# Performance work log

Measured on AMD Instinct MI355X. Metric: run time of the kernel, lower is better.

Reference implementation:

```python
import jax, jax.numpy as jnp
import numpy as np

ETYPES = ((0, 2), (4, 6))  # per-metapath edge-type indices into the doubled r_vec table
ALPHA = 3.0


def celu3(x):
    return jax.nn.celu(x, alpha=ALPHA)


def cmul(a, b):
    # complex multiply, last dim = (real, imag)
    re = a[..., 0] * b[..., 0] - a[..., 1] * b[..., 1]
    im = a[..., 0] * b[..., 1] + a[..., 1] * b[..., 0]
    return jnp.stack([re, im], axis=-1)


def setup_inputs() -> dict:
    key = jax.random.key(0)
    ks = jax.random.split(key, 10)
    N, H, heads, M, E, P = 50000, 64, 4, 2, 250000, 3
    R, FH = 4, 128
    D = heads * H
    return {
        "features": jax.random.normal(ks[0], (N, H), jnp.float32),
        "r_vec": jax.random.normal(ks[1], (R, H // 2, 2), jnp.float32),
        "attn1_w": jax.random.normal(ks[2], (heads, H), jnp.float32) * 0.1,
        "attn2": jax.random.normal(ks[3], (1, heads, H), jnp.float32) * 0.1,
        "fw1": jax.random.normal(ks[4], (2 * FH, D), jnp.float32) * 0.05,
        "fb1": jnp.zeros((2 * FH,), jnp.float32),
        "fw2": jax.random.normal(ks[5], (FH, 2 * FH), jnp.float32) * 0.05,
        "fb2": jnp.zeros((FH,), jnp.float32),
        "fw3": jax.random.normal(ks[6], (1, FH), jnp.float32) * 0.05,
        "instances": jax.random.randint(ks[7], (M, E, P), 0, N, jnp.int32),
    }


def reference(features, r_vec, attn1_w, attn2, fw1, fb1, fw2, fb2, fw3, instances):
    N, H = features.shape
    M, E, P = instances.shape
    heads = attn1_w.shape[0]
    # unit-modulus rotations + conjugates: [2R, H/2, 2], even=r, odd=conj(r)
    rv = r_vec / jnp.linalg.norm(r_vec, axis=2, keepdims=True)
    conj = rv * jnp.array([1.0, -1.0], rv.dtype)
    rv2 = jnp.stack([rv, conj], axis=1).reshape(-1, H // 2, 2)

    per_path = []
    for m in range(M):
        inst = instances[m]  # [E, P]
        # backward cumulative rotation: final_r[i] = prod_{j>=i} r_{etype[j]}, final_r[P-1]=1
        ident = jnp.stack([jnp.ones(H // 2, rv.dtype), jnp.zeros(H // 2, rv.dtype)], axis=-1)
        frs = [ident]
        for i in range(P - 2, -1, -1):
            frs.insert(0, cmul(frs[0], rv2[ETYPES[m][i]]))
        fr = jnp.stack(frs)  # [P, H/2, 2]
        # gather features along metapath and rotate (last position rotated by identity)
        edata = features[inst].reshape(E, P, H // 2, 2)
        rot = cmul(edata, fr[None])
        me = jnp.mean(rot.reshape(E, P, H), axis=1)  # [E, H]
        se = celu3(me) * jax.nn.sigmoid(me)  # gated metapath embedding
        eft = celu3(se)  # same across heads in original (tiled)
        seg = inst[:, 0]  # target node per instance
        a1 = celu3(features[seg] @ attn1_w.T)  # [E, heads]
        a2 = jnp.einsum('eh,kh->ek', eft, attn2[0])  # [E, heads]
        a = celu3(a1 + a2)
        # segment softmax over each node's instance set
        amax = jax.ops.segment_max(a, seg, num_segments=N)
        ex = jnp.exp(a - amax[seg])
        den = jax.ops.segment_sum(ex, seg, num_segments=N)
        attn = ex / den[seg]  # [E, heads]
        hsum = jax.ops.segment_sum(attn[:, :, None] * eft[:, None, :], seg, num_segments=N)
        per_path.append(celu3(hsum).reshape(N, heads * H))  # empty nodes -> 0

    z = jnp.stack(per_path, axis=1)  # [N, M, D]
    t = celu3(z @ fw1.T + fb1)
    t = celu3(t @ fw2.T + fb2)
    w = (t @ fw3.T).mean(axis=0)  # [M, 1]
    beta = jax.nn.softmax(w, axis=0)
    out = (beta * z).sum(axis=1)  # [N, D]
    return out
```

## Files before the change

kernel.cpp:

```cpp
#include <hip/hip_runtime.h>
#include <hip/hip_bf16.h>

typedef unsigned short u16;
typedef unsigned int   u32;
typedef short bf16x8 __attribute__((ext_vector_type(8)));
typedef float f32x4  __attribute__((ext_vector_type(4)));

#define CAP 64

__device__ inline float b2f(u16 u){ return __builtin_bit_cast(float, (u32)u << 16); }
__device__ inline u16 f2b(float f){
  u32 x = __builtin_bit_cast(u32, f);
  x += 0x7fffu + ((x >> 16) & 1u);
  return (u16)(x >> 16);
}
__device__ inline u32 pk2(float lo, float hi){
  float2 f; f.x = lo; f.y = hi;
  __hip_bfloat162 h = __float22bfloat162_rn(f);
  u32 r; __builtin_memcpy(&r, &h, 4);
  return r;
}
__device__ inline void up2(u32 u, float& lo, float& hi){
  lo = __builtin_bit_cast(float, u << 16);
  hi = __builtin_bit_cast(float, u & 0xffff0000u);
}
__device__ inline float fexp(float x){ return __expf(x); }
__device__ inline float celu3(float x){
  return x > 0.f ? x : 3.f * (__expf(x * (1.f/3.f)) - 1.f);
}
__device__ inline float sigm(float x){ return 1.f / (1.f + __expf(-x)); }

__global__ __launch_bounds__(256) void conv_kernel(
    const float* __restrict__ src, u16* __restrict__ dst, int n8)
{
  int i = blockIdx.x * 256 + threadIdx.x;
  if (i >= n8) return;
  float4 a = ((const float4*)src)[2*i], b = ((const float4*)src)[2*i + 1];
  uint4 o;
  o.x = pk2(a.x, a.y);
  o.y = pk2(a.z, a.w);
  o.z = pk2(b.x, b.y);
  o.w = pk2(b.z, b.w);
  ((uint4*)dst)[i] = o;
}

__global__ __launch_bounds__(256) void a1_kernel(
    const float* __restrict__ feat, const float* __restrict__ attn1,
    u16* __restrict__ featb, float* __restrict__ a1c, int N)
{
  __shared__ float w1s[256];
  int t = threadIdx.x;
  w1s[t] = attn1[t];
  __syncthreads();
  int g = t >> 4, l = t & 15;
  int n = blockIdx.x * 16 + g;
  if (n >= N) return;
  float4 x = ((const float4*)feat)[(size_t)n*16 + l];
  uint2 o;
  o.x = pk2(x.x, x.y);
  o.y = pk2(x.z, x.w);
  ((uint2*)featb)[(size_t)n*16 + l] = o;
  float d[4];
  #pragma unroll
  for (int k = 0; k < 4; ++k){
    int wb = k*64 + l*4;
    d[k] = x.x*w1s[wb] + x.y*w1s[wb+1] + x.z*w1s[wb+2] + x.w*w1s[wb+3];
  }
  #pragma unroll
  for (int off = 8; off; off >>= 1){
    #pragma unroll
    for (int k = 0; k < 4; ++k) d[k] += __shfl_xor(d[k], off);
  }
  if (l == 0){
    float4 av;
    av.x = celu3(d[0]); av.y = celu3(d[1]);
    av.z = celu3(d[2]); av.w = celu3(d[3]);
    ((float4*)a1c)[n] = av;
  }
}

__global__ void fr_kernel(const float* __restrict__ rvec, float* __restrict__ fr){
  int c = threadIdx.x;
  if (c >= 32) return;
  for (int m = 0; m < 2; ++m){
    float ar = rvec[(2*m)*64 + c*2],   ai = rvec[(2*m)*64 + c*2 + 1];
    float br = rvec[(2*m+1)*64 + c*2], bi = rvec[(2*m+1)*64 + c*2 + 1];
    float na = rsqrtf(ar*ar + ai*ai); ar *= na; ai *= na;
    float nb = rsqrtf(br*br + bi*bi); br *= nb; bi *= nb;
    float* f = fr + m*128;
    f[c*2]        = br*ar - bi*ai;
    f[c*2 + 1]    = br*ai + bi*ar;
    f[64 + c*2]   = br;
    f[64 + c*2+1] = bi;
  }
}

__global__ __launch_bounds__(256) void edge_kernel(
    const u16* __restrict__ featb, const int* __restrict__ inst,
    const float* __restrict__ fr, const float* __restrict__ a1c,
    const float* __restrict__ attn2, u16* __restrict__ eft,
    float* __restrict__ a_ws, int* __restrict__ cnt, int* __restrict__ bucket,
    int E, int N)
{
  __shared__ float frs[128];
  __shared__ float w2s[256];
  int m = blockIdx.y;
  int t = threadIdx.x;
  if (t < 128) frs[t] = fr[m*128 + t];
  w2s[t] = attn2[t];
  __syncthreads();

  int g = t >> 4, l = t & 15;
  int e = blockIdx.x * 16 + g;
  if (e >= E) return;
  int base = (m*E + e)*3;
  int i0 = inst[base], i1 = inst[base+1], i2 = inst[base+2];

  const uint2* fb = (const uint2*)featb;
  uint2 v0 = fb[(size_t)i0*16 + l];
  uint2 v1 = fb[(size_t)i1*16 + l];
  uint2 v2 = fb[(size_t)i2*16 + l];
  float f0[4], f1[4], f2v[4];
  up2(v0.x, f0[0], f0[1]); up2(v0.y, f0[2], f0[3]);
  up2(v1.x, f1[0], f1[1]); up2(v1.y, f1[2], f1[3]);
  up2(v2.x, f2v[0], f2v[1]); up2(v2.y, f2v[2], f2v[3]);

  float4 R0 = *(const float4*)&frs[4*l];
  float4 R1 = *(const float4*)&frs[64 + 4*l];

  float mre0 = (f0[0]*R0.x - f0[1]*R0.y + f1[0]*R1.x - f1[1]*R1.y + f2v[0]) * (1.f/3.f);
  float mim0 = (f0[0]*R0.y + f0[1]*R0.x + f1[0]*R1.y + f1[1]*R1.x + f2v[1]) * (1.f/3.f);
  float mre1 = (f0[2]*R0.z - f0[3]*R0.w + f1[2]*R1.z - f1[3]*R1.w + f2v[2]) * (1.f/3.f);
  float mim1 = (f0[2]*R0.w + f0[3]*R0.z + f1[2]*R1.w + f1[3]*R1.z + f2v[3]) * (1.f/3.f);

  float ef[4], s;
  s = celu3(mre0) * sigm(mre0); ef[0] = celu3(s);
  s = celu3(mim0) * sigm(mim0); ef[1] = celu3(s);
  s = celu3(mre1) * sigm(mre1); ef[2] = celu3(s);
  s = celu3(mim1) * sigm(mim1); ef[3] = celu3(s);

  uint2 uo;
  uo.x = pk2(ef[0], ef[1]);
  uo.y = pk2(ef[2], ef[3]);
  ((uint2*)eft)[(size_t)(m*E + e)*16 + l] = uo;

  float d2[4];
  #pragma unroll
  for (int k = 0; k < 4; ++k){
    int wb = k*64 + l*4;
    d2[k] = ef[0]*w2s[wb] + ef[1]*w2s[wb+1] + ef[2]*w2s[wb+2] + ef[3]*w2s[wb+3];
  }
  #pragma unroll
  for (int off = 8; off; off >>= 1){
    #pragma unroll
    for (int k = 0; k < 4; ++k) d2[k] += __shfl_xor(d2[k], off);
  }
  if (l == 0){
    float4 a1v = ((const float4*)a1c)[i0];
    float4 av;
    av.x = celu3(a1v.x + d2[0]);
    av.y = celu3(a1v.y + d2[1]);
    av.z = celu3(a1v.z + d2[2]);
    av.w = celu3(a1v.w + d2[3]);
    ((float4*)a_ws)[m*E + e] = av;
    int pos = atomicAdd(&cnt[m*N + i0], 1);
    if (pos < CAP) bucket[(size_t)(m*N + i0)*CAP + pos] = e;
  }
}

__global__ __launch_bounds__(256) void seg_kernel(
    const float* __restrict__ a_ws, const u16* __restrict__ eft,
    const int* __restrict__ cnt, const int* __restrict__ bucket,
    u16* __restrict__ z, int E, int N)
{
  int m = blockIdx.y;
  int n = blockIdx.x * 4 + (threadIdx.x >> 6);
  if (n >= N) return;
  int lane = threadIdx.x & 63;
  int sidx = m*N + n;
  int deg = cnt[sidx]; if (deg > CAP) deg = CAP;

  float h0=0.f, h1=0.f, h2=0.f, h3=0.f;
  float d0=0.f, d1=0.f, d2=0.f, d3=0.f;
  if (deg > 0){
    const int* bk = bucket + (size_t)sidx * CAP;
    size_t ebase = (size_t)m * E;

    int e = (lane < deg) ? bk[lane] : 0;
    float w0 = 0.f, w1 = 0.f, w2 = 0.f, w3 = 0.f;
    if (lane < deg){
      float4 av = ((const float4*)a_ws)[ebase + e];
      w0 = fexp(av.x); w1 = fexp(av.y); w2 = fexp(av.z); w3 = fexp(av.w);
    }

    const u16* ep = eft + ebase*64;
    for (int j = 0; j < deg; ++j){
      int   ej  = __shfl(e,  j);
      float a0j = __shfl(w0, j), a1j = __shfl(w1, j);
      float a2j = __shfl(w2, j), a3j = __shfl(w3, j);
      float ev = b2f(ep[(size_t)ej*64 + lane]);
      h0 += a0j*ev; h1 += a1j*ev; h2 += a2j*ev; h3 += a3j*ev;
      d0 += a0j;    d1 += a1j;    d2 += a2j;    d3 += a3j;
    }
    h0 /= d0; h1 /= d1; h2 /= d2; h3 /= d3;
  }
  u16* zr = z + (size_t)sidx*256 + lane;
  zr[0]   = f2b(celu3(h0));
  zr[64]  = f2b(celu3(h1));
  zr[128] = f2b(celu3(h2));
  zr[192] = f2b(celu3(h3));
}

__global__ __launch_bounds__(256, 4) void mlp_kernel(
    const u16* __restrict__ z, const u16* __restrict__ fw1b, const float* __restrict__ fb1,
    const u16* __restrict__ fw2b, const float* __restrict__ fb2, const float* __restrict__ fw3,
    float* __restrict__ wacc, int rows, int N)
{
  __shared__ u16 buf[64][264];
  __shared__ float fw3s[128];
  __shared__ float sArr[64];
  u16 (*t2t)[136] = (u16 (*)[136])&buf[0][0];
  int tid = threadIdx.x;
  int row0 = blockIdx.x * 64;

  if (tid < 128) fw3s[tid] = fw3[tid];

  const uint4* zg = (const uint4*)z;
  #pragma unroll
  for (int it = 0; it < 8; ++it){
    int idx = it*256 + tid;
    int row = idx >> 5;
    int c8  = idx & 31;
    uint4 v = make_uint4(0u,0u,0u,0u);
    int gr = row0 + row;
    if (gr < rows) v = zg[(size_t)gr*32 + c8];
    *(uint4*)&buf[row][c8*8] = v;
  }
  __syncthreads();

  int wv = tid >> 6, lane = tid & 63, lr = lane & 15, quad = lane >> 4;
  f32x4 zero4 = {0.f, 0.f, 0.f, 0.f};

  f32x4 acc[4][4];
  #pragma unroll
  for (int a = 0; a < 4; ++a)
    #pragma unroll
    for (int b = 0; b < 4; ++b) acc[a][b] = zero4;

  const u16* wb1 = fw1b + (size_t)(wv*64 + lr)*256 + quad*8;
  bf16x8 bfr[4], bnx[4];
  #pragma unroll
  for (int nt = 0; nt < 4; ++nt) bfr[nt] = *(const bf16x8*)(wb1 + nt*16*256);
  #pragma unroll
  for (int ks = 0; ks < 8; ++ks){
    if (ks < 7){
      #pragma unroll
      for (int nt = 0; nt < 4; ++nt)
        bnx[nt] = *(const bf16x8*)(wb1 + nt*16*256 + (ks+1)*32);
    }
    #pragma unroll
    for (int mt = 0; mt < 4; ++mt){
      bf16x8 af = *(const bf16x8*)&buf[mt*16 + lr][ks*32 + quad*8];
      #pragma unroll
      for (int nt = 0; nt < 4; ++nt)
        acc[mt][nt] = __builtin_amdgcn_mfma_f32_16x16x32_bf16(af, bfr[nt], acc[mt][nt], 0, 0, 0);
    }
    #pragma unroll
    for (int nt = 0; nt < 4; ++nt) bfr[nt] = bnx[nt];
  }
  __syncthreads();
  #pragma unroll
  for (int nt = 0; nt < 4; ++nt){
    int col = wv*64 + nt*16 + lr;
    float bias = fb1[col];
    #pragma unroll
    for (int mt = 0; mt < 4; ++mt)
      #pragma unroll
      for (int ri = 0; ri < 4; ++ri){
        int row = mt*16 + quad*4 + ri;
        buf[row][col] = f2b(celu3(acc[mt][nt][ri] + bias));
      }
  }
  __syncthreads();

  f32x4 acc2[4][2];
  #pragma unroll
  for (int a = 0; a < 4; ++a){ acc2[a][0] = zero4; acc2[a][1] = zero4; }
  const u16* wb2 = fw2b + (size_t)(wv*32 + lr)*256 + quad*8;
  bf16x8 cfr[2], cnx[2];
  cfr[0] = *(const bf16x8*)(wb2);
  cfr[1] = *(const bf16x8*)(wb2 + 16*256);
  #pragma unroll
  for (int ks = 0; ks < 8; ++ks){
    if (ks < 7){
      cnx[0] = *(const bf16x8*)(wb2 + (ks+1)*32);
      cnx[1] = *(const bf16x8*)(wb2 + 16*256 + (ks+1)*32);
    }
    #pragma unroll
    for (int mt = 0; mt < 4; ++mt){
      bf16x8 af = *(const bf16x8*)&buf[mt*16 + lr][ks*32 + quad*8];
      acc2[mt][0] = __builtin_amdgcn_mfma_f32_16x16x32_bf16(af, cfr[0], acc2[mt][0], 0, 0, 0);
      acc2[mt][1] = __builtin_amdgcn_mfma_f32_16x16x32_bf16(af, cfr[1], acc2[mt][1], 0, 0, 0);
    }
    cfr[0] = cnx[0]; cfr[1] = cnx[1];
  }
  __syncthreads();
  #pragma unroll
  for (int nt = 0; nt < 2; ++nt){
    int col = wv*32 + nt*16 + lr;
    float bias = fb2[col];
    #pragma unroll
    for (int mt = 0; mt < 4; ++mt)
      #pragma unroll
      for (int ri = 0; ri < 4; ++ri)
        t2t[mt*16 + quad*4 + ri][col] = f2b(celu3(acc2[mt][nt][ri] + bias));
  }
  __syncthreads();

  int r = tid >> 2, q = tid & 3;
  float p = 0.f;
  #pragma unroll
  for (int j = 0; j < 32; ++j){
    int jj = q*32 + j;
    p += b2f(t2t[r][jj]) * fw3s[jj];
  }
  p += __shfl_xor(p, 1);
  p += __shfl_xor(p, 2);
  if (q == 0) sArr[r] = p;
  __syncthreads();

  if (tid < 64){
    int gr = row0 + tid;
    float s  = (gr < rows) ? sArr[tid] : 0.f;
    float s0 = (gr < N) ? s : 0.f;
    float s1 = (gr < N) ? 0.f : s;
    #pragma unroll
    for (int off = 32; off; off >>= 1){
      s0 += __shfl_xor(s0, off);
      s1 += __shfl_xor(s1, off);
    }
    if (tid == 0){
      atomicAdd(&wacc[0], s0);
      atomicAdd(&wacc[1], s1);
    }
  }
}

__global__ void beta_kernel(float* __restrict__ wacc, float invN){
  if (threadIdx.x == 0 && blockIdx.x == 0){
    float w0 = wacc[0]*invN, w1 = wacc[1]*invN;
    float mx = fmaxf(w0, w1);
    float e0 = __expf(w0 - mx), e1 = __expf(w1 - mx);
    float s = e0 + e1;
    wacc[2] = e0 / s;
    wacc[3] = e1 / s;
  }
}

__global__ __launch_bounds__(256) void out_kernel(
    const u16* __restrict__ z, const float* __restrict__ wacc,
    float* __restrict__ out, int total)
{
  int idx = blockIdx.x * 256 + threadIdx.x;
  if (idx*8 >= total) return;
  float b0 = wacc[2], b1 = wacc[3];
  uint4 u0 = ((const uint4*)z)[idx];
  uint4 u1 = ((const uint4*)z)[(total >> 3) + idx];
  float a0,a1v,c0,c1;
  float4 o;
  up2(u0.x, a0, a1v); up2(u1.x, c0, c1);
  o.x = b0*a0 + b1*c0; o.y = b0*a1v + b1*c1;
  up2(u0.y, a0, a1v); up2(u1.y, c0, c1);
  o.z = b0*a0 + b1*c0; o.w = b0*a1v + b1*c1;
  ((float4*)out)[idx*2] = o;
  up2(u0.z, a0, a1v); up2(u1.z, c0, c1);
  o.x = b0*a0 + b1*c0; o.y = b0*a1v + b1*c1;
  up2(u0.w, a0, a1v); up2(u1.w, c0, c1);
  o.z = b0*a0 + b1*c0; o.w = b0*a1v + b1*c1;
  ((float4*)out)[idx*2 + 1] = o;
}

extern "C" void kernel_launch(void* const* d_in, const int* in_sizes, int n_in,
                              void* d_out, int out_size, void* d_ws, size_t ws_size,
                              hipStream_t stream)
{
  (void)n_in; (void)out_size; (void)ws_size;
  const float* feat  = (const float*)d_in[0];
  const float* rvec  = (const float*)d_in[1];
  const float* attn1 = (const float*)d_in[2];
  const float* attn2 = (const float*)d_in[3];
  const float* fw1   = (const float*)d_in[4];
  const float* fb1   = (const float*)d_in[5];
  const float* fw2   = (const float*)d_in[6];
  const float* fb2   = (const float*)d_in[7];
  const float* fw3   = (const float*)d_in[8];
  const int*   inst  = (const int*)d_in[9];

  int N = in_sizes[0] / 64;
  int E = in_sizes[9] / 6;

  char* ws = (char*)d_ws;
  u16*   z      = (u16*)ws;                            size_t zB = (size_t)2*N*256*2;
  u16*   eft    = (u16*)(ws + zB);                     size_t eB = (size_t)2*E*64*2;
  float* a_ws   = (float*)(ws + zB + eB);              size_t aB = (size_t)2*E*4*4;
  int*   bucket = (int*)(ws + zB + eB + aB);           size_t bB = (size_t)2*N*CAP*4;
  int*   cnt    = (int*)(ws + zB + eB + aB + bB);      size_t cB = (size_t)2*N*4;
  u16*   featb  = (u16*)(ws + zB + eB + aB + bB + cB); size_t fB = (size_t)N*64*2;
  float* a1c    = (float*)(ws + zB + eB + aB + bB + cB + fB);  size_t a1B = (size_t)N*4*4;
  u16*   fw1b   = (u16*)(ws + zB + eB + aB + bB + cB + fB + a1B);
  u16*   fw2b   = fw1b + 256*256;
  float* fr     = (float*)(fw2b + 128*256);
  float* wacc   = fr + 256;

  hipMemsetAsync(cnt, 0, cB, stream);
  hipMemsetAsync(wacc, 0, 2*sizeof(float), stream);

  a1_kernel<<<(N + 15)/16, 256, 0, stream>>>(feat, attn1, featb, a1c, N);
  conv_kernel<<<(256*256/8 + 255)/256, 256, 0, stream>>>(fw1, fw1b, 256*256/8);
  conv_kernel<<<(128*256/8 + 255)/256, 256, 0, stream>>>(fw2, fw2b, 128*256/8);
  fr_kernel<<<1, 64, 0, stream>>>(rvec, fr);
  edge_kernel<<<dim3((E + 15)/16, 2), 256, 0, stream>>>(
      featb, inst, fr, a1c, attn2, eft, a_ws, cnt, bucket, E, N);
  seg_kernel<<<dim3((N + 3)/4, 2), 256, 0, stream>>>(a_ws, eft, cnt, bucket, z, E, N);
  mlp_kernel<<<(2*N + 63)/64, 256, 0, stream>>>(z, fw1b, fb1, fw2b, fb2, fw3, wacc, 2*N, N);
  beta_kernel<<<1, 64, 0, stream>>>(wacc, 1.f/(float)N);
  out_kernel<<<((N*256/8) + 255)/256, 256, 0, stream>>>(z, wacc, (float*)d_out, N*256);
}
```

Before: 302.2 us.

## Shrink MLP tiles to 32 rows, fuse fw3 dot into registers, spread atomics

The MLP kernel now processes 32 rows per block instead of 64 and targets 6 blocks per CU. It drops the software prefetch of weight fragments and computes the final fw3 dot product straight from MFMA accumulators with shuffle reductions, which removes the second LDS round-trip and two barriers. The global atomics are spread over 64 slots per metapath, and beta_kernel reduces those slots. The cost is twice as many blocks, each reloading the weights from L2, and less latency hiding on the weight loads.

After: 310.2 us. 2.6% more time.

```diff
diff --git a/kernel.cpp b/kernel.cpp
--- a/kernel.cpp
+++ b/kernel.cpp
@@ -211,23 +211,22 @@
   zr[192] = f2b(celu3(h3));
 }
 
-__global__ __launch_bounds__(256, 4) void mlp_kernel(
+__global__ __launch_bounds__(256, 6) void mlp_kernel(
     const u16* __restrict__ z, const u16* __restrict__ fw1b, const float* __restrict__ fb1,
     const u16* __restrict__ fw2b, const float* __restrict__ fb2, const float* __restrict__ fw3,
-    float* __restrict__ wacc, int rows, int N)
-{
-  __shared__ u16 buf[64][264];
+    float* __restrict__ waccP, int rows, int N)
+{
+  __shared__ u16 buf[32][264];
   __shared__ float fw3s[128];
-  __shared__ float sArr[64];
-  u16 (*t2t)[136] = (u16 (*)[136])&buf[0][0];
+  __shared__ float sPart[4][32];
   int tid = threadIdx.x;
-  int row0 = blockIdx.x * 64;
+  int row0 = blockIdx.x * 32;
 
   if (tid < 128) fw3s[tid] = fw3[tid];
 
   const uint4* zg = (const uint4*)z;
   #pragma unroll
-  for (int it = 0; it < 8; ++it){
+  for (int it = 0; it < 4; ++it){
     int idx = it*256 + tid;
     int row = idx >> 5;
     int c8  = idx & 31;
@@ -241,32 +240,26 @@
   int wv = tid >> 6, lane = tid & 63, lr = lane & 15, quad = lane >> 4;
   f32x4 zero4 = {0.f, 0.f, 0.f, 0.f};
 
-  f32x4 acc[4][4];
-  #pragma unroll
-  for (int a = 0; a < 4; ++a)
+  f32x4 acc[2][4];
+  #pragma unroll
+  for (int a = 0; a < 2; ++a)
     #pragma unroll
     for (int b = 0; b < 4; ++b) acc[a][b] = zero4;
 
   const u16* wb1 = fw1b + (size_t)(wv*64 + lr)*256 + quad*8;
-  bf16x8 bfr[4], bnx[4];
-  #pragma unroll
-  for (int nt = 0; nt < 4; ++nt) bfr[nt] = *(const bf16x8*)(wb1 + nt*16*256);
   #pragma unroll
   for (int ks = 0; ks < 8; ++ks){
-    if (ks < 7){
-      #pragma unroll
-      for (int nt = 0; nt < 4; ++nt)
-        bnx[nt] = *(const bf16x8*)(wb1 + nt*16*256 + (ks+1)*32);
-    }
-    #pragma unroll
-    for (int mt = 0; mt < 4; ++mt){
+    bf16x8 bfr[4];
+    #pragma unroll
+    for (int nt = 0; nt < 4; ++nt)
+      bfr[nt] = *(const bf16x8*)(wb1 + nt*16*256 + ks*32);
+    #pragma unroll
+    for (int mt = 0; mt < 2; ++mt){
       bf16x8 af = *(const bf16x8*)&buf[mt*16 + lr][ks*32 + quad*8];
       #pragma unroll
       for (int nt = 0; nt < 4; ++nt)
         acc[mt][nt] = __builtin_amdgcn_mfma_f32_16x16x32_bf16(af, bfr[nt], acc[mt][nt], 0, 0, 0);
     }
-    #pragma unroll
-    for (int nt = 0; nt < 4; ++nt) bfr[nt] = bnx[nt];
   }
   __syncthreads();
   #pragma unroll
@@ -274,7 +267,7 @@
     int col = wv*64 + nt*16 + lr;
     float bias = fb1[col];
     #pragma unroll
-    for (int mt = 0; mt < 4; ++mt)
+    for (int mt = 0; mt < 2; ++mt)
       #pragma unroll
       for (int ri = 0; ri < 4; ++ri){
         int row = mt*16 + quad*4 + ri;
@@ -283,77 +276,89 @@
   }
   __syncthreads();
 
-  f32x4 acc2[4][2];
-  #pragma unroll
-  for (int a = 0; a < 4; ++a){ acc2[a][0] = zero4; acc2[a][1] = zero4; }
+  f32x4 acc2[2][2];
+  #pragma unroll
+  for (int a = 0; a < 2; ++a){ acc2[a][0] = zero4; acc2[a][1] = zero4; }
   const u16* wb2 = fw2b + (size_t)(wv*32 + lr)*256 + quad*8;
-  bf16x8 cfr[2], cnx[2];
-  cfr[0] = *(const bf16x8*)(wb2);
-  cfr[1] = *(const bf16x8*)(wb2 + 16*256);
   #pragma unroll
   for (int ks = 0; ks < 8; ++ks){
-    if (ks < 7){
-      cnx[0] = *(const bf16x8*)(wb2 + (ks+1)*32);
-      cnx[1] = *(const bf16x8*)(wb2 + 16*256 + (ks+1)*32);
-    }
-    #pragma unroll
-    for (int mt = 0; mt < 4; ++mt){
+    bf16x8 cfr[2];
+    cfr[0] = *(const bf16x8*)(wb2 + ks*32);
+    cfr[1] = *(const bf16x8*)(wb2 + 16*256 + ks*32);
+    #pragma unroll
+    for (int mt = 0; mt < 2; ++mt){
       bf16x8 af = *(const bf16x8*)&buf[mt*16 + lr][ks*32 + quad*8];
       acc2[mt][0] = __builtin_amdgcn_mfma_f32_16x16x32_bf16(af, cfr[0], acc2[mt][0], 0, 0, 0);
       acc2[mt][1] = __builtin_amdgcn_mfma_f32_16x16x32_bf16(af, cfr[1], acc2[mt][1], 0, 0, 0);
     }
-    cfr[0] = cnx[0]; cfr[1] = cnx[1];
-  }
-  __syncthreads();
+  }
+
+  float ps[2][4];
+  #pragma unroll
+  for (int mt = 0; mt < 2; ++mt)
+    #pragma unroll
+    for (int ri = 0; ri < 4; ++ri) ps[mt][ri] = 0.f;
   #pragma unroll
   for (int nt = 0; nt < 2; ++nt){
     int col = wv*32 + nt*16 + lr;
     float bias = fb2[col];
-    #pragma unroll
-    for (int mt = 0; mt < 4; ++mt)
+    float w3 = fw3s[col];
+    #pragma unroll
+    for (int mt = 0; mt < 2; ++mt)
       #pragma unroll
       for (int ri = 0; ri < 4; ++ri)
-        t2t[mt*16 + quad*4 + ri][col] = f2b(celu3(acc2[mt][nt][ri] + bias));
-  }
-  __syncthreads();
-
-  int r = tid >> 2, q = tid & 3;
-  float p = 0.f;
-  #pragma unroll
-  for (int j = 0; j < 32; ++j){
-    int jj = q*32 + j;
-    p += b2f(t2t[r][jj]) * fw3s[jj];
-  }
-  p += __shfl_xor(p, 1);
-  p += __shfl_xor(p, 2);
-  if (q == 0) sArr[r] = p;
-  __syncthreads();
-
-  if (tid < 64){
+        ps[mt][ri] += celu3(acc2[mt][nt][ri] + bias) * w3;
+  }
+  #pragma unroll
+  for (int off = 8; off; off >>= 1)
+    #pragma unroll
+    for (int mt = 0; mt < 2; ++mt)
+      #pragma unroll
+      for (int ri = 0; ri < 4; ++ri)
+        ps[mt][ri] += __shfl_xor(ps[mt][ri], off);
+  if (lr == 0){
+    #pragma unroll
+    for (int mt = 0; mt < 2; ++mt)
+      #pragma unroll
+      for (int ri = 0; ri < 4; ++ri)
+        sPart[wv][mt*16 + quad*4 + ri] = ps[mt][ri];
+  }
+  __syncthreads();
+
+  if (tid < 32){
+    float s = sPart[0][tid] + sPart[1][tid] + sPart[2][tid] + sPart[3][tid];
     int gr = row0 + tid;
-    float s  = (gr < rows) ? sArr[tid] : 0.f;
+    if (gr >= rows) s = 0.f;
     float s0 = (gr < N) ? s : 0.f;
     float s1 = (gr < N) ? 0.f : s;
     #pragma unroll
-    for (int off = 32; off; off >>= 1){
+    for (int off = 16; off; off >>= 1){
       s0 += __shfl_xor(s0, off);
       s1 += __shfl_xor(s1, off);
     }
     if (tid == 0){
-      atomicAdd(&wacc[0], s0);
-      atomicAdd(&wacc[1], s1);
+      int slot = blockIdx.x & 63;
+      atomicAdd(&waccP[slot],      s0);
+      atomicAdd(&waccP[64 + slot], s1);
     }
   }
 }
 
 __global__ void beta_kernel(float* __restrict__ wacc, float invN){
-  if (threadIdx.x == 0 && blockIdx.x == 0){
-    float w0 = wacc[0]*invN, w1 = wacc[1]*invN;
+  int t = threadIdx.x;
+  float s0 = wacc[t], s1 = wacc[64 + t];
+  #pragma unroll
+  for (int off = 32; off; off >>= 1){
+    s0 += __shfl_xor(s0, off);
+    s1 += __shfl_xor(s1, off);
+  }
+  if (t == 0){
+    float w0 = s0*invN, w1 = s1*invN;
     float mx = fmaxf(w0, w1);
     float e0 = __expf(w0 - mx), e1 = __expf(w1 - mx);
     float s = e0 + e1;
-    wacc[2] = e0 / s;
-    wacc[3] = e1 / s;
+    wacc[128] = e0 / s;
+    wacc[129] = e1 / s;
   }
 }
 
@@ -363,7 +368,7 @@
 {
   int idx = blockIdx.x * 256 + threadIdx.x;
   if (idx*8 >= total) return;
-  float b0 = wacc[2], b1 = wacc[3];
+  float b0 = wacc[128], b1 = wacc[129];
   uint4 u0 = ((const uint4*)z)[idx];
   uint4 u1 = ((const uint4*)z)[(total >> 3) + idx];
   float a0,a1v,c0,c1;
@@ -413,7 +418,7 @@
   float* wacc   = fr + 256;
 
   hipMemsetAsync(cnt, 0, cB, stream);
-  hipMemsetAsync(wacc, 0, 2*sizeof(float), stream);
+  hipMemsetAsync(wacc, 0, 128*sizeof(float), stream);
 
   a1_kernel<<<(N + 15)/16, 256, 0, stream>>>(feat, attn1, featb, a1c, N);
   conv_kernel<<<(256*256/8 + 255)/256, 256, 0, stream>>>(fw1, fw1b, 256*256/8);
@@ -422,7 +427,7 @@
   edge_kernel<<<dim3((E + 15)/16, 2), 256, 0, stream>>>(
       featb, inst, fr, a1c, attn2, eft, a_ws, cnt, bucket, E, N);
   seg_kernel<<<dim3((N + 3)/4, 2), 256, 0, stream>>>(a_ws, eft, cnt, bucket, z, E, N);
-  mlp_kernel<<<(2*N + 63)/64, 256, 0, stream>>>(z, fw1b, fb1, fw2b, fb2, fw3, wacc, 2*N, N);
+  mlp_kernel<<<(2*N + 31)/32, 256, 0, stream>>>(z, fw1b, fb1, fw2b, fb2, fw3, wacc, 2*N, N);
   beta_kernel<<<1, 64, 0, stream>>>(wacc, 1.f/(float)N);
   out_kernel<<<((N*256/8) + 255)/256, 256, 0, stream>>>(z, wacc, (float*)d_out, N*256);
 }
```
